# Kernel tuning notes

Measured on AMD Instinct MI355X. Metric: run time of the kernel, lower is better.

The kernel has to match this reference:

```python
import jax, jax.numpy as jnp
import numpy as np

PI = 3.1415926
CHAINS = [[0, 2, 5, 8, 11], [0, 1, 4, 7, 10], [0, 3, 6, 9, 12, 15], [9, 14, 17, 19, 21], [9, 13, 16, 18, 20]]
NUM_JOINTS = 22
CTX = 512
B = 131072


def setup_inputs() -> dict:
    key = jax.random.key(0)
    k_ctx, k_w0, k_b0, k_w, k_b = jax.random.split(key, 5)
    context_vec = jax.random.normal(k_ctx, (B, CTX), dtype=jnp.float32)
    # root linear: context_size -> 3
    W0 = jax.random.normal(k_w0, (CTX, 3), dtype=jnp.float32) * 0.02
    b0 = jax.random.normal(k_b0, (3,), dtype=jnp.float32) * 0.02
    # non-root linears: (context_size + 3) -> 3, stacked per joint index (row 0 unused)
    W = jax.random.normal(k_w, (NUM_JOINTS, CTX + 3, 3), dtype=jnp.float32) * 0.02
    b = jax.random.normal(k_b, (NUM_JOINTS, 3), dtype=jnp.float32) * 0.02
    return {"context_vec": context_vec, "W0": W0, "b0": b0, "W": W, "b": b}


def reference(context_vec, W0, b0, W, b):
    # Sequential per-joint tiny linears along kinematic chains (do_all_parent=False):
    # each child consumes [context, parent_joint(3)] -> 3, then tanh * PI.
    joints = [None] * NUM_JOINTS
    joints[0] = jnp.tanh(context_vec @ W0 + b0) * PI  # [B, 3]
    for chain in CHAINS:
        for j in range(1, len(chain)):
            jid = chain[j]
            inp = jnp.concatenate([context_vec, joints[chain[j - 1]]], axis=-1)  # [B, CTX+3]
            joints[jid] = jnp.tanh(inp @ W[jid] + b[jid]) * PI
    return jnp.concatenate(joints, axis=-1)  # [B, 3*NUM_JOINTS]
```

## Files before the change

### kernel.cpp

```cpp
#include <hip/hip_runtime.h>
#include <cstdint>
#include <cstddef>


#define CTXD 512
#define NCOL 66
#define KT   16
#define NT   5
#define ROWS_PER_BLOCK 128
#define LDS_STRIDE 67

typedef __attribute__((ext_vector_type(8))) short  short8;
typedef __attribute__((ext_vector_type(4))) float  f32x4;

__device__ __forceinline__ unsigned short f2bf(float x) {
  unsigned u = __float_as_uint(x);
  unsigned r = (u + 0x7FFFu + ((u >> 16) & 1u)) >> 16;
  return (unsigned short)r;
}

__device__ __forceinline__ float tanhpi(float x) {
  float t = exp2f(x * 2.885390081777927f);
  return 3.1415926f - 6.2831852f * __builtin_amdgcn_rcpf(t + 1.0f);
}

__global__ void prep_wfrag(const float* __restrict__ W0,
                           const float* __restrict__ W,
                           unsigned short* __restrict__ wf) {
  int idx = blockIdx.x * blockDim.x + threadIdx.x;
  if (idx >= KT * NT * 64 * 8) return;
  int j    = idx & 7;
  int lane = (idx >> 3) & 63;
  int rest = idx >> 9;
  int nt   = rest % NT;
  int kt   = rest / NT;
  int k    = kt * 32 + (lane >> 4) * 8 + j;
  int col  = nt * 16 + (lane & 15);
  float v = 0.f;
  if (col < 3)          v = W0[k * 3 + col];
  else if (col < NCOL)  v = W[(col / 3) * (515 * 3) + k * 3 + (col % 3)];
  wf[idx] = f2bf(v);
}

__global__ __launch_bounds__(256) void hdl_main(
    const float* __restrict__ ctx,
    const float* __restrict__ b0,
    const float* __restrict__ W,
    const float* __restrict__ bflat,
    const unsigned short* __restrict__ wf,
    float* __restrict__ out)
{
  __shared__ float lds[ROWS_PER_BLOCK * LDS_STRIDE];

  const int tid  = threadIdx.x;
  const int lane = tid & 63;
  const int wave = tid >> 6;
  const int r16  = lane & 15;
  const int kg   = lane >> 4;
  const long blockRow = (long)blockIdx.x * ROWS_PER_BLOCK;

  f32x4 acc[2][NT] = {};

  float bias[NT];
#pragma unroll
  for (int n = 0; n < NT; ++n) {
    int col = n * 16 + r16;
    bias[n] = (col < 3) ? b0[col] : ((col < NCOL) ? bflat[col] : 0.f);
  }

  const float* a0 = ctx + (blockRow + wave * 32 + r16) * CTXD + kg * 8;

  for (int kt = 0; kt < KT; ++kt) {
    short8 bfr[NT];
#pragma unroll
    for (int n = 0; n < NT; ++n)
      bfr[n] = *(const short8*)(wf + (size_t)((kt * NT + n) * 64 + lane) * 8);

#pragma unroll
    for (int m = 0; m < 2; ++m) {
      const float* ap = a0 + (size_t)m * 16 * CTXD + kt * 32;
      float4 f0 = *(const float4*)(ap);
      float4 f1 = *(const float4*)(ap + 4);
      short8 afr;
      afr[0] = (short)f2bf(f0.x); afr[1] = (short)f2bf(f0.y);
      afr[2] = (short)f2bf(f0.z); afr[3] = (short)f2bf(f0.w);
      afr[4] = (short)f2bf(f1.x); afr[5] = (short)f2bf(f1.y);
      afr[6] = (short)f2bf(f1.z); afr[7] = (short)f2bf(f1.w);
#pragma unroll
      for (int n = 0; n < NT; ++n)
        acc[m][n] = __builtin_amdgcn_mfma_f32_16x16x32_bf16(
            afr, bfr[n], acc[m][n], 0, 0, 0);
    }
  }

#pragma unroll
  for (int m = 0; m < 2; ++m) {
#pragma unroll
    for (int n = 0; n < NT; ++n) {
      int col = n * 16 + r16;
      if (col < NCOL) {
        int rb = wave * 32 + m * 16 + kg * 4;
#pragma unroll
        for (int q = 0; q < 4; ++q)
          lds[(rb + q) * LDS_STRIDE + col] = acc[m][n][q] + bias[n];
      }
    }
  }
  __syncthreads();

  if (tid < ROWS_PER_BLOCK) {
    float* row = lds + tid * LDS_STRIDE;
    float J[22][3];
#pragma unroll
    for (int c = 0; c < 3; ++c) J[0][c] = tanhpi(row[c]);

    constexpr int EP[21] = {0,2,5,8, 0,1,4,7, 0,3,6,9,12, 9,14,17,19, 9,13,16,18};
    constexpr int EC[21] = {2,5,8,11, 1,4,7,10, 3,6,9,12,15, 14,17,19,21, 13,16,18,20};
#pragma unroll
    for (int e = 0; e < 21; ++e) {
      const int p  = EP[e];
      const int ch = EC[e];
      const float* wp = W + ch * 1545 + 1536;
#pragma unroll
      for (int c = 0; c < 3; ++c) {
        float s = row[3 * ch + c];
        s += J[p][0] * wp[c] + J[p][1] * wp[3 + c] + J[p][2] * wp[6 + c];
        J[ch][c] = tanhpi(s);
      }
    }
#pragma unroll
    for (int jj = 0; jj < 22; ++jj)
#pragma unroll
      for (int c = 0; c < 3; ++c) row[3 * jj + c] = J[jj][c];
  }
  __syncthreads();

  const size_t outBase = (size_t)blockRow * NCOL;
  for (int i = tid; i < ROWS_PER_BLOCK * NCOL; i += 256) {
    int r = i / NCOL;
    int c = i - r * NCOL;
    out[outBase + i] = lds[r * LDS_STRIDE + c];
  }
}

extern "C" void kernel_launch(void* const* d_in, const int* in_sizes, int n_in,
                              void* d_out, int out_size, void* d_ws, size_t ws_size,
                              hipStream_t stream) {
  const float* ctx  = (const float*)d_in[0];
  const float* W0   = (const float*)d_in[1];
  const float* b0   = (const float*)d_in[2];
  const float* W    = (const float*)d_in[3];
  const float* bfl  = (const float*)d_in[4];
  unsigned short* wf = (unsigned short*)d_ws;

  int prep_elems = KT * NT * 64 * 8;
  hipLaunchKernelGGL(prep_wfrag, dim3((prep_elems + 255) / 256), dim3(256), 0,
                     stream, W0, W, wf);

  int nrows = out_size / NCOL;
  hipLaunchKernelGGL(hdl_main, dim3(nrows / ROWS_PER_BLOCK), dim3(256), 0,
                     stream, ctx, b0, W, bfl, wf, (float*)d_out);
}
```

Measured before the change: 76.13 us.

## Stage context tiles through LDS with direct global-to-LDS loads and packed bf16 convert

Replaces per-lane strided global float4 loads of the context with coalesced global_load_lds transfers into a per-wave LDS staging buffer, 64 columns at a time, then reads MFMA A-fragments from LDS. The fp32-to-bf16 conversion uses the hardware packed v_cvt_pk_bf16_f32 instruction instead of manual integer rounding. A launch bound of 4 blocks per SM is also added. Each chunk waits on vmcnt(0) with no double buffering, so load latency is not overlapped with the MFMAs. Reusing the same LDS for staging and the epilogue needs an extra barrier.

```diff
diff --git a/kernel.cpp b/kernel.cpp
--- a/kernel.cpp
+++ b/kernel.cpp
@@ -7,7 +7,8 @@
 #define NCOL 66
 #define KT   16
 #define NT   5
-#define ROWS_PER_BLOCK 128
+#define NCH  8
+#define RPB  128
 #define LDS_STRIDE 67
 
 typedef __attribute__((ext_vector_type(8))) short  short8;
@@ -15,8 +16,13 @@
 
 __device__ __forceinline__ unsigned short f2bf(float x) {
   unsigned u = __float_as_uint(x);
-  unsigned r = (u + 0x7FFFu + ((u >> 16) & 1u)) >> 16;
-  return (unsigned short)r;
+  return (unsigned short)((u + 0x7FFFu + ((u >> 16) & 1u)) >> 16);
+}
+
+__device__ __forceinline__ unsigned cvt2(float a, float b) {
+  unsigned r;
+  asm("v_cvt_pk_bf16_f32 %0, %1, %2" : "=v"(r) : "v"(a), "v"(b));
+  return r;
 }
 
 __device__ __forceinline__ float tanhpi(float x) {
@@ -42,7 +48,7 @@
   wf[idx] = f2bf(v);
 }
 
-__global__ __launch_bounds__(256) void hdl_main(
+__global__ __launch_bounds__(256, 4) void hdl_main(
     const float* __restrict__ ctx,
     const float* __restrict__ b0,
     const float* __restrict__ W,
@@ -50,14 +56,14 @@
     const unsigned short* __restrict__ wf,
     float* __restrict__ out)
 {
-  __shared__ float lds[ROWS_PER_BLOCK * LDS_STRIDE];
+  __shared__ float smem[RPB * LDS_STRIDE];
 
   const int tid  = threadIdx.x;
   const int lane = tid & 63;
   const int wave = tid >> 6;
   const int r16  = lane & 15;
   const int kg   = lane >> 4;
-  const long blockRow = (long)blockIdx.x * ROWS_PER_BLOCK;
+  const long blockRow = (long)blockIdx.x * RPB;
 
   f32x4 acc[2][NT] = {};
 
@@ -68,30 +74,49 @@
     bias[n] = (col < 3) ? b0[col] : ((col < NCOL) ? bflat[col] : 0.f);
   }
 
-  const float* a0 = ctx + (blockRow + wave * 32 + r16) * CTXD + kg * 8;
+  float* stage = smem + wave * 2048;
+  const float* srcBase =
+      ctx + (blockRow + wave * 32 + (lane >> 4)) * (long)CTXD + (lane & 15) * 4;
 
-  for (int kt = 0; kt < KT; ++kt) {
-    short8 bfr[NT];
+  for (int c = 0; c < NCH; ++c) {
 #pragma unroll
-    for (int n = 0; n < NT; ++n)
-      bfr[n] = *(const short8*)(wf + (size_t)((kt * NT + n) * 64 + lane) * 8);
+    for (int j = 0; j < 8; ++j) {
+      const float* s = srcBase + (size_t)j * 4 * CTXD + c * 64;
+      __builtin_amdgcn_global_load_lds(
+          (const __attribute__((address_space(1))) void*)s,
+          (__attribute__((address_space(3))) void*)(stage + j * 256),
+          16, 0, 0);
+    }
+    asm volatile("s_waitcnt vmcnt(0)" ::: "memory");
 
 #pragma unroll
-    for (int m = 0; m < 2; ++m) {
-      const float* ap = a0 + (size_t)m * 16 * CTXD + kt * 32;
-      float4 f0 = *(const float4*)(ap);
-      float4 f1 = *(const float4*)(ap + 4);
-      short8 afr;
-      afr[0] = (short)f2bf(f0.x); afr[1] = (short)f2bf(f0.y);
-      afr[2] = (short)f2bf(f0.z); afr[3] = (short)f2bf(f0.w);
-      afr[4] = (short)f2bf(f1.x); afr[5] = (short)f2bf(f1.y);
-      afr[6] = (short)f2bf(f1.z); afr[7] = (short)f2bf(f1.w);
+    for (int t = 0; t < 2; ++t) {
+      const int kt = c * 2 + t;
+      short8 bfr[NT];
 #pragma unroll
       for (int n = 0; n < NT; ++n)
-        acc[m][n] = __builtin_amdgcn_mfma_f32_16x16x32_bf16(
-            afr, bfr[n], acc[m][n], 0, 0, 0);
+        bfr[n] = *(const short8*)(wf + (size_t)((kt * NT + n) * 64 + lane) * 8);
+
+#pragma unroll
+      for (int m = 0; m < 2; ++m) {
+        const float* fp = stage + (m * 16 + r16) * 64 + t * 32 + kg * 8;
+        float4 f0 = *(const float4*)(fp);
+        float4 f1 = *(const float4*)(fp + 4);
+        union { short8 s; unsigned u[4]; } A;
+        A.u[0] = cvt2(f0.x, f0.y);
+        A.u[1] = cvt2(f0.z, f0.w);
+        A.u[2] = cvt2(f1.x, f1.y);
+        A.u[3] = cvt2(f1.z, f1.w);
+#pragma unroll
+        for (int n = 0; n < NT; ++n)
+          acc[m][n] = __builtin_amdgcn_mfma_f32_16x16x32_bf16(
+              A.s, bfr[n], acc[m][n], 0, 0, 0);
+      }
     }
+    asm volatile("" ::: "memory");
   }
+
+  __syncthreads();
 
 #pragma unroll
   for (int m = 0; m < 2; ++m) {
@@ -102,17 +127,17 @@
         int rb = wave * 32 + m * 16 + kg * 4;
 #pragma unroll
         for (int q = 0; q < 4; ++q)
-          lds[(rb + q) * LDS_STRIDE + col] = acc[m][n][q] + bias[n];
+          smem[(rb + q) * LDS_STRIDE + col] = acc[m][n][q] + bias[n];
       }
     }
   }
   __syncthreads();
 
-  if (tid < ROWS_PER_BLOCK) {
-    float* row = lds + tid * LDS_STRIDE;
+  if (tid < RPB) {
+    float* row = smem + tid * LDS_STRIDE;
     float J[22][3];
 #pragma unroll
-    for (int c = 0; c < 3; ++c) J[0][c] = tanhpi(row[c]);
+    for (int cc = 0; cc < 3; ++cc) J[0][cc] = tanhpi(row[cc]);
 
     constexpr int EP[21] = {0,2,5,8, 0,1,4,7, 0,3,6,9,12, 9,14,17,19, 9,13,16,18};
     constexpr int EC[21] = {2,5,8,11, 1,4,7,10, 3,6,9,12,15, 14,17,19,21, 13,16,18,20};
@@ -122,24 +147,24 @@
       const int ch = EC[e];
       const float* wp = W + ch * 1545 + 1536;
 #pragma unroll
-      for (int c = 0; c < 3; ++c) {
-        float s = row[3 * ch + c];
-        s += J[p][0] * wp[c] + J[p][1] * wp[3 + c] + J[p][2] * wp[6 + c];
-        J[ch][c] = tanhpi(s);
+      for (int cc = 0; cc < 3; ++cc) {
+        float s = row[3 * ch + cc];
+        s += J[p][0] * wp[cc] + J[p][1] * wp[3 + cc] + J[p][2] * wp[6 + cc];
+        J[ch][cc] = tanhpi(s);
       }
     }
 #pragma unroll
     for (int jj = 0; jj < 22; ++jj)
 #pragma unroll
-      for (int c = 0; c < 3; ++c) row[3 * jj + c] = J[jj][c];
+      for (int cc = 0; cc < 3; ++cc) row[3 * jj + cc] = J[jj][cc];
   }
   __syncthreads();
 
   const size_t outBase = (size_t)blockRow * NCOL;
-  for (int i = tid; i < ROWS_PER_BLOCK * NCOL; i += 256) {
+  for (int i = tid; i < RPB * NCOL; i += 256) {
     int r = i / NCOL;
-    int c = i - r * NCOL;
-    out[outBase + i] = lds[r * LDS_STRIDE + c];
+    int cc = i - r * NCOL;
+    out[outBase + i] = smem[r * LDS_STRIDE + cc];
   }
 }
 
@@ -158,6 +183,6 @@
                      stream, W0, W, wf);
 
   int nrows = out_size / NCOL;
-  hipLaunchKernelGGL(hdl_main, dim3(nrows / ROWS_PER_BLOCK), dim3(256), 0,
+  hipLaunchKernelGGL(hdl_main, dim3(nrows / RPB), dim3(256), 0,
                      stream, ctx, b0, W, bfl, wf, (float*)d_out);
 }
```

After: 64.04 us. -15.9%, faster.
